# Kernel tuning notes

Hardware: AMD Instinct MI355X
Metric: run time of the kernel (lower is better)

Reference implementation:

```python
import jax, jax.numpy as jnp
import numpy as np

NUM_USERS = 100000
NUM_ITEMS = 100000
D = 128
L = 8
FV = 64
FH = 64
B = 8192
FC_IN = FV * D + FH * L  # 8704


def setup_inputs() -> dict:
    key = jax.random.key(0)
    ks = jax.random.split(key, 16)
    s = 0.05  # weight scale for sane magnitudes
    return {
        "user_id": jax.random.randint(ks[0], (B,), 0, NUM_USERS),
        "seq_L": jax.random.randint(ks[1], (B, L), 0, NUM_ITEMS),
        "item_id": jax.random.randint(ks[2], (B,), 0, NUM_ITEMS),
        "Q": jax.random.normal(ks[3], (NUM_ITEMS, D), jnp.float32) * s,
        "P": jax.random.normal(ks[4], (NUM_USERS, D), jnp.float32) * s,
        "Qp": jax.random.normal(ks[5], (NUM_ITEMS, 2 * D), jnp.float32) * s,
        "b_item": jax.random.normal(ks[6], (NUM_ITEMS,), jnp.float32) * s,
        "Wv": jax.random.normal(ks[7], (FV, L), jnp.float32) * s,
        "bv": jax.random.normal(ks[8], (FV,), jnp.float32) * s,
        "Wh": jax.random.normal(ks[9], (L, FH, L, D), jnp.float32) * s,
        "bh": jax.random.normal(ks[10], (L, FH), jnp.float32) * s,
        "Wfc": jax.random.normal(ks[11], (D, FC_IN), jnp.float32) * s,
        "bfc": jax.random.normal(ks[12], (D,), jnp.float32) * s,
    }


def reference(user_id, seq_L, item_id, Q, P, Qp, b_item, Wv, bv, Wh, bh, Wfc, bfc):
    # seq embeddings: [B, L, D]
    x = Q[seq_L]
    # vertical conv: kernel (L,1) -> out [B, Fv, D], then relu + flatten
    out_v = jax.nn.relu(jnp.einsum("bld,fl->bfd", x, Wv) + bv[None, :, None])
    out_v = out_v.reshape(out_v.shape[0], FV * D)  # [B, Fv*D]
    # horizontal conv blocks h = 1..L (static loop over kernel heights)
    h_feats = []
    for h in range(1, L + 1):
        w = Wh[h - 1, :, :h, :]  # [Fh, h, D]
        # sliding windows over sequence: [B, L-h+1, h, D]
        win = jnp.stack([x[:, j : j + h] for j in range(L - h + 1)], axis=1)
        o = jnp.einsum("bjhd,fhd->bjf", win, w) + bh[h - 1]  # [B, L-h+1, Fh]
        h_feats.append(jnp.max(jax.nn.relu(o), axis=1))  # [B, Fh]
    out_h = jnp.concatenate(h_feats, axis=1)  # [B, Fh*L]
    combined = jnp.concatenate([out_v, out_h], axis=1)  # [B, Fv*D + Fh*L]
    # (dropout p=0 / inference -> identity)
    z = jax.nn.relu(combined @ Wfc.T + bfc)  # [B, D]
    x2 = jnp.concatenate([z, P[user_id]], axis=1)  # [B, 2D]
    score = jnp.einsum("bd,bd->b", x2, Qp[item_id]) + b_item[item_id]
    return score
```

## Files before the change

### kernel.cpp

```cpp
#include <hip/hip_runtime.h>
#include <hip/hip_bf16.h>
#include <cstdint>
#include <cstddef>

typedef short bf16x8 __attribute__((ext_vector_type(8)));
typedef short bf16x4 __attribute__((ext_vector_type(4)));
typedef float f32x4  __attribute__((ext_vector_type(4)));

#define MFMA16(A, B, C) __builtin_amdgcn_mfma_f32_16x16x32_bf16(A, B, C, 0, 0, 0)

constexpr int XSTR = 1032;
constexpr int BSTR = 520;
constexpr size_t WS_FC   = (size_t)2176 * 1024;
constexpr size_t WS_BOTH = WS_FC + (size_t)576 * 1024;

__device__ __forceinline__ unsigned short f2bf(float x) {
    unsigned u = __float_as_uint(x);
    unsigned r = u + 0x7fffu + ((u >> 16) & 1u);
    return (unsigned short)(r >> 16);
}
__device__ __forceinline__ float bf2f(unsigned short h) {
    return __uint_as_float(((unsigned)h) << 16);
}
__device__ __forceinline__ unsigned pkbf(float a, float b) {
    __hip_bfloat162 h = __float22bfloat162_rn(make_float2(a, b));
    return *reinterpret_cast<unsigned*>(&h);
}
__device__ __forceinline__ bf16x8 load8_f32(const float* __restrict__ s) {
    float4 a = *(const float4*)s;
    float4 b = *(const float4*)(s + 4);
    bf16x8 r;
    r[0]=(short)f2bf(a.x); r[1]=(short)f2bf(a.y); r[2]=(short)f2bf(a.z); r[3]=(short)f2bf(a.w);
    r[4]=(short)f2bf(b.x); r[5]=(short)f2bf(b.y); r[6]=(short)f2bf(b.z); r[7]=(short)f2bf(b.w);
    return r;
}

template<int MODE>
__device__ __forceinline__ bf16x8 fc_bfrag(const unsigned short* __restrict__ wfcb,
                                           const float* __restrict__ Wfc,
                                           int kg, int ntile, int lane)
{
    if constexpr (MODE >= 1) {
        return *(const bf16x8*)(wfcb + (((size_t)(kg * 8 + ntile)) << 9) + lane * 8);
    } else {
        const float* s = Wfc + (size_t)(ntile * 16 + (lane & 15)) * 8704
                             + kg * 32 + (lane >> 4) * 8;
        return load8_f32(s);
    }
}
template<int MODE>
__device__ __forceinline__ bf16x8 wh_bfrag(const unsigned short* __restrict__ whb,
                                           const float* __restrict__ Wh,
                                           int H, int kstep, int ntile, int lane)
{
    if constexpr (MODE == 2) {
        return *(const bf16x8*)(whb +
            (((size_t)(8 * H * (H - 1) + kstep * 4 + ntile)) << 9) + lane * 8);
    } else {
        const int k = kstep * 32 + (lane >> 4) * 8;
        const float* s = Wh + ((((size_t)(H - 1) * 64 + ntile * 16 + (lane & 15)) * 8
                               + (k >> 7)) * 128 + (k & 127));
        return load8_f32(s);
    }
}

__global__ __launch_bounds__(256)
void caser_prep(const float* __restrict__ Wfc, const float* __restrict__ Wh,
                unsigned short* __restrict__ wfcb, unsigned short* __restrict__ whb,
                int nfrag)
{
    const int tid = blockIdx.x * 256 + threadIdx.x;
    const int lane = tid & 63, frag = tid >> 6;
    if (frag >= nfrag) return;
    if (frag < 2176) {
        const int kg = frag >> 3, nt = frag & 7;
        bf16x8 v = fc_bfrag<0>(nullptr, Wfc, kg, nt, lane);
        *(bf16x8*)(wfcb + ((size_t)frag << 9) + lane * 8) = v;
    } else {
        const int f2 = frag - 2176;
        int h = 1;
        while (f2 >= 8 * h * (h + 1)) ++h;
        const int fl = f2 - 8 * h * (h - 1);
        const int nt = fl & 3, kstep = fl >> 2;
        bf16x8 v = wh_bfrag<0>(nullptr, Wh, h, kstep, nt, lane);
        *(bf16x8*)(whb + ((size_t)f2 << 9) + lane * 8) = v;
    }
}

template<int H, int PP, int MODE>
__device__ __forceinline__ void hconv_compute(
    const unsigned short* __restrict__ xs,
    const unsigned short* __restrict__ whb, const float* __restrict__ Wh,
    const float* __restrict__ bh,
    int m, int nt4, int lane, int laneA, float mx[4])
{
    constexpr int NJ = 9 - H;
    constexpr int NJS = (PP == 0) ? ((NJ + 1) / 2) : (NJ / 2);
    if constexpr (NJS > 0) {
        f32x4 C[NJS] = {};
        const unsigned short* xbase = xs + m * 16 * XSTR + laneA;
        #pragma unroll
        for (int kstep = 0; kstep < 4 * H; ++kstep) {
            const int hp = kstep >> 2, d0 = (kstep & 3) * 32;
            bf16x8 B = wh_bfrag<MODE>(whb, Wh, H, kstep, nt4, lane);
            #pragma unroll
            for (int idx = 0; idx < NJS; ++idx) {
                const int j = PP + 2 * idx;
                bf16x8 A = *(const bf16x8*)(xbase + (j + hp) * 128 + d0);
                C[idx] = MFMA16(A, B, C[idx]);
            }
        }
        const float bhv = bh[(H - 1) * 64 + nt4 * 16 + (lane & 15)];
        #pragma unroll
        for (int idx = 0; idx < NJS; ++idx)
            #pragma unroll
            for (int r = 0; r < 4; ++r)
                mx[r] = fmaxf(mx[r], fmaxf(C[idx][r] + bhv, 0.f));
    }
}

template<int H, int MODE>
__device__ __forceinline__ void hstep(
    const unsigned short* __restrict__ xs, unsigned short* __restrict__ feat,
    float* __restrict__ candc,
    const unsigned short* __restrict__ whb, const float* __restrict__ Wh,
    const float* __restrict__ bh,
    int t, int lane, int laneA, int hm, int hn4, int pj)
{
    float mx[4] = {};
    if (pj == 0) hconv_compute<H, 0, MODE>(xs, whb, Wh, bh, hm, hn4, lane, laneA, mx);
    else         hconv_compute<H, 1, MODE>(xs, whb, Wh, bh, hm, hn4, lane, laneA, mx);
    #pragma unroll
    for (int r = 0; r < 4; ++r)
        candc[pj * 2176 + (hm * 16 + (lane >> 4) * 4 + r) * 68 +
              hn4 * 16 + (lane & 15)] = mx[r];
    __syncthreads();
    {
        const int s = t >> 5, f0 = (t & 31) * 2;
        float a0 = fmaxf(candc[s * 68 + f0],     candc[2176 + s * 68 + f0]);
        float a1 = fmaxf(candc[s * 68 + f0 + 1], candc[2176 + s * 68 + f0 + 1]);
        *(unsigned*)(feat + s * BSTR + (H - 1) * 64 + f0) = pkbf(a0, a1);
    }
}

template<int MODE>
__global__ __launch_bounds__(1024, 1)
void caser_main(const int* __restrict__ user_id,
                const int* __restrict__ seq,
                const int* __restrict__ item_id,
                const float* __restrict__ Q,
                const float* __restrict__ Pmat,
                const float* __restrict__ Qp,
                const float* __restrict__ b_item,
                const float* __restrict__ Wv,
                const float* __restrict__ bv,
                const float* __restrict__ Wh,
                const float* __restrict__ bh,
                const float* __restrict__ Wfc,
                const float* __restrict__ bfc,
                const unsigned short* __restrict__ wfcb,
                const unsigned short* __restrict__ whb,
                float* __restrict__ out)
{
    __shared__ unsigned short xs[32 * XSTR];
    __shared__ unsigned short fbuf[2 * 32 * BSTR];
    __shared__ float cand[2 * 32 * 68];
    __shared__ float wv_s[576];

    const int t = threadIdx.x;
    const int lane = t & 63;
    const int w = t >> 6;
    const int b0 = blockIdx.x * 32;
    const int laneA = (lane & 15) * XSTR + (lane >> 4) * 8;
    const int laneB = (lane & 15) * BSTR + (lane >> 4) * 8;
    const int kh = w & 3, ng = w >> 2;
    const int hm = w & 1, hn4 = (w >> 1) & 3, pj = (w >> 3) & 1;

    if (t < 576) wv_s[t] = (t < 512) ? Wv[t] : bv[t - 512];
    #pragma unroll
    for (int k = 0; k < 8; ++k) {
        const int idx = t + k * 1024;
        const int i = idx & 31;
        const int l = (idx >> 5) & 7;
        const int s = idx >> 8;
        const int it = seq[(b0 + s) * 8 + l];
        float4 v = *(const float4*)(Q + (size_t)it * 128 + i * 4);
        uint2 pk;
        pk.x = pkbf(v.x, v.y);
        pk.y = pkbf(v.z, v.w);
        *(uint2*)(xs + s * XSTR + l * 128 + i * 4) = pk;
    }
    __syncthreads();

    const int sv = t & 31, dq = t >> 5;
    float xr[8][4];
    #pragma unroll
    for (int l = 0; l < 8; ++l) {
        bf16x4 v = *(const bf16x4*)(xs + sv * XSTR + l * 128 + dq * 4);
        #pragma unroll
        for (int i = 0; i < 4; ++i) xr[l][i] = bf2f((unsigned short)v[i]);
    }

    f32x4 FCC[2][2] = {};

    uint2 vc[4];
    #define VCONV_HALF(hc_)                                                    \
        {                                                                      \
            _Pragma("unroll")                                                  \
            for (int fl = 0; fl < 4; ++fl) {                                   \
                const int f = (hc_) * 4 + fl;                                  \
                const float bvv = wv_s[512 + f];                               \
                float acc[4];                                                  \
                _Pragma("unroll")                                              \
                for (int i = 0; i < 4; ++i) acc[i] = bvv;                      \
                _Pragma("unroll")                                              \
                for (int l = 0; l < 8; ++l) {                                  \
                    const float wl = wv_s[f * 8 + l];                          \
                    _Pragma("unroll")                                          \
                    for (int i = 0; i < 4; ++i)                                \
                        acc[i] = fmaf(xr[l][i], wl, acc[i]);                   \
                }                                                              \
                vc[fl].x = pkbf(fmaxf(acc[0], 0.f), fmaxf(acc[1], 0.f));       \
                vc[fl].y = pkbf(fmaxf(acc[2], 0.f), fmaxf(acc[3], 0.f));       \
            }                                                                  \
        }
    #define VSTORE(buf_)                                                       \
        {                                                                      \
            unsigned short* fb = fbuf + (buf_) * (32 * BSTR);                  \
            _Pragma("unroll")                                                  \
            for (int fl = 0; fl < 4; ++fl)                                     \
                *(uint2*)(fb + sv * BSTR + fl * 128 + dq * 4) = vc[fl];        \
        }

    bf16x8 BF0[4], BF1[4];
    #pragma unroll
    for (int ks = 0; ks < 4; ++ks) {
        const int kg = kh * 4 + ks;
        BF0[ks] = fc_bfrag<MODE>(wfcb, Wfc, kg, ng * 2,     lane);
        BF1[ks] = fc_bfrag<MODE>(wfcb, Wfc, kg, ng * 2 + 1, lane);
    }
    VCONV_HALF(0);
    VSTORE(0);
    __syncthreads();

    #pragma unroll 1
    for (int hc = 0; hc < 16; ++hc) {
        {
            const unsigned short* fb = fbuf + (hc & 1) * (32 * BSTR);
            #pragma unroll
            for (int ks = 0; ks < 4; ++ks) {
                const int kl = kh * 4 + ks;
                bf16x8 A0 = *(const bf16x8*)(fb + laneB + kl * 32);
                bf16x8 A1 = *(const bf16x8*)(fb + 16 * BSTR + laneB + kl * 32);
                FCC[0][0] = MFMA16(A0, BF0[ks], FCC[0][0]);
                FCC[0][1] = MFMA16(A0, BF1[ks], FCC[0][1]);
                FCC[1][0] = MFMA16(A1, BF0[ks], FCC[1][0]);
                FCC[1][1] = MFMA16(A1, BF1[ks], FCC[1][1]);
            }
        }
        if (hc < 15) {
            #pragma unroll
            for (int ks = 0; ks < 4; ++ks) {
                const int kg = (hc + 1) * 16 + kh * 4 + ks;
                BF0[ks] = fc_bfrag<MODE>(wfcb, Wfc, kg, ng * 2,     lane);
                BF1[ks] = fc_bfrag<MODE>(wfcb, Wfc, kg, ng * 2 + 1, lane);
            }
            VCONV_HALF(hc + 1);
            VSTORE((hc + 1) & 1);
        }
        __syncthreads();
    }
    #undef VCONV_HALF
    #undef VSTORE

    unsigned short* feat = fbuf;
    float* candA = cand;
    float* candB = (float*)(fbuf + 32 * BSTR);
    hstep<1, MODE>(xs, feat, candA, whb, Wh, bh, t, lane, laneA, hm, hn4, pj);
    hstep<2, MODE>(xs, feat, candB, whb, Wh, bh, t, lane, laneA, hm, hn4, pj);
    hstep<3, MODE>(xs, feat, candA, whb, Wh, bh, t, lane, laneA, hm, hn4, pj);
    hstep<4, MODE>(xs, feat, candB, whb, Wh, bh, t, lane, laneA, hm, hn4, pj);
    hstep<5, MODE>(xs, feat, candA, whb, Wh, bh, t, lane, laneA, hm, hn4, pj);
    hstep<6, MODE>(xs, feat, candB, whb, Wh, bh, t, lane, laneA, hm, hn4, pj);
    hstep<7, MODE>(xs, feat, candA, whb, Wh, bh, t, lane, laneA, hm, hn4, pj);
    hstep<8, MODE>(xs, feat, candB, whb, Wh, bh, t, lane, laneA, hm, hn4, pj);

    #pragma unroll
    for (int kgi = 0; kgi < 4; ++kgi) {
        const int kg = 256 + kh * 4 + kgi;
        BF0[kgi] = fc_bfrag<MODE>(wfcb, Wfc, kg, ng * 2,     lane);
        BF1[kgi] = fc_bfrag<MODE>(wfcb, Wfc, kg, ng * 2 + 1, lane);
    }
    __syncthreads();

    #pragma unroll
    for (int kgi = 0; kgi < 4; ++kgi) {
        const int kloc = kh * 4 + kgi;
        bf16x8 A0 = *(const bf16x8*)(feat + laneB + kloc * 32);
        bf16x8 A1 = *(const bf16x8*)(feat + 16 * BSTR + laneB + kloc * 32);
        FCC[0][0] = MFMA16(A0, BF0[kgi], FCC[0][0]);
        FCC[0][1] = MFMA16(A0, BF1[kgi], FCC[0][1]);
        FCC[1][0] = MFMA16(A1, BF0[kgi], FCC[1][0]);
        FCC[1][1] = MFMA16(A1, BF1[kgi], FCC[1][1]);
    }

    float* zbuf4 = (float*)xs;
    #pragma unroll
    for (int m = 0; m < 2; ++m)
        #pragma unroll
        for (int nt = 0; nt < 2; ++nt)
            #pragma unroll
            for (int r = 0; r < 4; ++r)
                zbuf4[kh * (32 * 132) + (m * 16 + (lane >> 4) * 4 + r) * 132 +
                      ng * 32 + nt * 16 + (lane & 15)] = FCC[m][nt][r];
    __syncthreads();
    {
        const int s = t >> 5, l32 = t & 31, o0 = l32 * 4;
        const int b = b0 + s;
        const int item = item_id[b];
        const int user = user_id[b];
        const float* qp = Qp + (size_t)item * 256;
        const float* pu = Pmat + (size_t)user * 128;
        float acc2 = 0.f;
        #pragma unroll
        for (int i = 0; i < 4; ++i) {
            float z = zbuf4[s * 132 + o0 + i]
                    + zbuf4[1 * (32 * 132) + s * 132 + o0 + i]
                    + zbuf4[2 * (32 * 132) + s * 132 + o0 + i]
                    + zbuf4[3 * (32 * 132) + s * 132 + o0 + i]
                    + bfc[o0 + i];
            z = fmaxf(z, 0.f);
            acc2 = fmaf(z, qp[o0 + i], acc2);
        }
        #pragma unroll
        for (int i = 0; i < 4; ++i)
            acc2 = fmaf(pu[o0 + i], qp[128 + o0 + i], acc2);
        acc2 += __shfl_xor(acc2, 1, 32);
        acc2 += __shfl_xor(acc2, 2, 32);
        acc2 += __shfl_xor(acc2, 4, 32);
        acc2 += __shfl_xor(acc2, 8, 32);
        acc2 += __shfl_xor(acc2, 16, 32);
        if (l32 == 0) out[b] = acc2 + b_item[item];
    }
}

extern "C" void kernel_launch(void* const* d_in, const int* in_sizes, int n_in,
                              void* d_out, int out_size, void* d_ws, size_t ws_size,
                              hipStream_t stream)
{
    const int*   user_id = (const int*)  d_in[0];
    const int*   seq     = (const int*)  d_in[1];
    const int*   item_id = (const int*)  d_in[2];
    const float* Q       = (const float*)d_in[3];
    const float* Pmat    = (const float*)d_in[4];
    const float* Qp      = (const float*)d_in[5];
    const float* b_item  = (const float*)d_in[6];
    const float* Wv      = (const float*)d_in[7];
    const float* bv      = (const float*)d_in[8];
    const float* Wh      = (const float*)d_in[9];
    const float* bh      = (const float*)d_in[10];
    const float* Wfc     = (const float*)d_in[11];
    const float* bfc     = (const float*)d_in[12];
    float* out = (float*)d_out;

    unsigned short* wfcb = (unsigned short*)d_ws;
    unsigned short* whb  = wfcb + WS_FC / 2;

    if (ws_size >= WS_BOTH) {
        hipLaunchKernelGGL(caser_prep, dim3(688), dim3(256), 0, stream,
                           Wfc, Wh, wfcb, whb, 2752);
        hipLaunchKernelGGL((caser_main<2>), dim3(256), dim3(1024), 0, stream,
                           user_id, seq, item_id, Q, Pmat, Qp, b_item,
                           Wv, bv, Wh, bh, Wfc, bfc, wfcb, whb, out);
    } else if (ws_size >= WS_FC) {
        hipLaunchKernelGGL(caser_prep, dim3(544), dim3(256), 0, stream,
                           Wfc, Wh, wfcb, whb, 2176);
        hipLaunchKernelGGL((caser_main<1>), dim3(256), dim3(1024), 0, stream,
                           user_id, seq, item_id, Q, Pmat, Qp, b_item,
                           Wv, bv, Wh, bh, Wfc, bfc, wfcb, whb, out);
    } else {
        hipLaunchKernelGGL((caser_main<0>), dim3(256), dim3(1024), 0, stream,
                           user_id, seq, item_id, Q, Pmat, Qp, b_item,
                           Wv, bv, Wh, bh, Wfc, bfc,
                           (const unsigned short*)nullptr, (const unsigned short*)nullptr, out);
    }
}
```

Baseline: 78.44 us.

## Prefetch horizontal-conv weight fragments and pin FC fragments in registers

Restructures the horizontal conv loop to load weight fragments one kernel row at a time into a double buffer, prefetching two rows ahead, and pins FC weight fragments with empty asm so their loads land before each barrier. It also swaps the thread-to-(sample, d) mapping in the vertical conv, changing the LDS access pattern. The launch bounds now ask for 4 blocks per CU, which constrains register allocation and may cause spills in exchange for potential occupancy.

```diff
diff --git a/kernel.cpp b/kernel.cpp
--- a/kernel.cpp
+++ b/kernel.cpp
@@ -25,6 +25,9 @@
 __device__ __forceinline__ unsigned pkbf(float a, float b) {
     __hip_bfloat162 h = __float22bfloat162_rn(make_float2(a, b));
     return *reinterpret_cast<unsigned*>(&h);
+}
+__device__ __forceinline__ void pin8(bf16x8 &v) {
+    asm volatile("" : "+v"(v));
 }
 __device__ __forceinline__ bf16x8 load8_f32(const float* __restrict__ s) {
     float4 a = *(const float4*)s;
@@ -99,15 +102,33 @@
     if constexpr (NJS > 0) {
         f32x4 C[NJS] = {};
         const unsigned short* xbase = xs + m * 16 * XSTR + laneA;
-        #pragma unroll
-        for (int kstep = 0; kstep < 4 * H; ++kstep) {
-            const int hp = kstep >> 2, d0 = (kstep & 3) * 32;
-            bf16x8 B = wh_bfrag<MODE>(whb, Wh, H, kstep, nt4, lane);
-            #pragma unroll
-            for (int idx = 0; idx < NJS; ++idx) {
-                const int j = PP + 2 * idx;
-                bf16x8 A = *(const bf16x8*)(xbase + (j + hp) * 128 + d0);
-                C[idx] = MFMA16(A, B, C[idx]);
+        bf16x8 Bq[2][4];
+        #pragma unroll
+        for (int q = 0; q < 4; ++q)
+            Bq[0][q] = wh_bfrag<MODE>(whb, Wh, H, q, nt4, lane);
+        if constexpr (H > 1) {
+            #pragma unroll
+            for (int q = 0; q < 4; ++q)
+                Bq[1][q] = wh_bfrag<MODE>(whb, Wh, H, 4 + q, nt4, lane);
+        }
+        #pragma unroll
+        for (int hp = 0; hp < H; ++hp) {
+            #pragma unroll
+            for (int q = 0; q < 4; ++q) pin8(Bq[hp & 1][q]);
+            #pragma unroll
+            for (int q = 0; q < 4; ++q) {
+                const int d0 = q * 32;
+                #pragma unroll
+                for (int idx = 0; idx < NJS; ++idx) {
+                    const int j = PP + 2 * idx;
+                    bf16x8 A = *(const bf16x8*)(xbase + (j + hp) * 128 + d0);
+                    C[idx] = MFMA16(A, Bq[hp & 1][q], C[idx]);
+                }
+            }
+            if (hp + 2 < H) {
+                #pragma unroll
+                for (int q = 0; q < 4; ++q)
+                    Bq[hp & 1][q] = wh_bfrag<MODE>(whb, Wh, H, (hp + 2) * 4 + q, nt4, lane);
             }
         }
         const float bhv = bh[(H - 1) * 64 + nt4 * 16 + (lane & 15)];
@@ -144,7 +165,7 @@
 }
 
 template<int MODE>
-__global__ __launch_bounds__(1024, 1)
+__global__ __launch_bounds__(1024, 4)
 void caser_main(const int* __restrict__ user_id,
                 const int* __restrict__ seq,
                 const int* __restrict__ item_id,
@@ -192,7 +213,7 @@
     }
     __syncthreads();
 
-    const int sv = t & 31, dq = t >> 5;
+    const int sv = t >> 5, dq = t & 31;
     float xr[8][4];
     #pragma unroll
     for (int l = 0; l < 8; ++l) {
@@ -231,6 +252,11 @@
             for (int fl = 0; fl < 4; ++fl)                                     \
                 *(uint2*)(fb + sv * BSTR + fl * 128 + dq * 4) = vc[fl];        \
         }
+    #define PIN_FRAGS()                                                        \
+        {                                                                      \
+            _Pragma("unroll")                                                  \
+            for (int ks = 0; ks < 4; ++ks) { pin8(BF0[ks]); pin8(BF1[ks]); }   \
+        }
 
     bf16x8 BF0[4], BF1[4];
     #pragma unroll
@@ -241,6 +267,7 @@
     }
     VCONV_HALF(0);
     VSTORE(0);
+    PIN_FRAGS();
     __syncthreads();
 
     #pragma unroll 1
@@ -267,6 +294,7 @@
             }
             VCONV_HALF(hc + 1);
             VSTORE((hc + 1) & 1);
+            PIN_FRAGS();
         }
         __syncthreads();
     }
@@ -291,7 +319,9 @@
         BF0[kgi] = fc_bfrag<MODE>(wfcb, Wfc, kg, ng * 2,     lane);
         BF1[kgi] = fc_bfrag<MODE>(wfcb, Wfc, kg, ng * 2 + 1, lane);
     }
+    PIN_FRAGS();
     __syncthreads();
+    #undef PIN_FRAGS
 
     #pragma unroll
     for (int kgi = 0; kgi < 4; ++kgi) {
```

After: 81.86 us. 1.04x slower.

## Halve block tile to 16 rows with 512 threads and repartition FC work

Applied to the files above, without the earlier changes.

Shrinks each block from 32 to 16 batch rows and from 1024 to 512 threads, doubling the grid to 512 blocks and allowing several blocks per CU through launch bounds. The FC GEMM is repartitioned so each wave owns one 16-column output tile over the full K, instead of splitting K across four waves. This removes the cross-wave K reduction through shared memory and lets bias and ReLU be fused at the accumulator. In exchange, B fragments are loaded inside the loop without prefetch, and the Wfc weights are read by twice as many blocks.

```diff
diff --git a/kernel.cpp b/kernel.cpp
--- a/kernel.cpp
+++ b/kernel.cpp
@@ -92,13 +92,13 @@
     const unsigned short* __restrict__ xs,
     const unsigned short* __restrict__ whb, const float* __restrict__ Wh,
     const float* __restrict__ bh,
-    int m, int nt4, int lane, int laneA, float mx[4])
+    int nt4, int lane, int laneA, float mx[4])
 {
     constexpr int NJ = 9 - H;
     constexpr int NJS = (PP == 0) ? ((NJ + 1) / 2) : (NJ / 2);
     if constexpr (NJS > 0) {
         f32x4 C[NJS] = {};
-        const unsigned short* xbase = xs + m * 16 * XSTR + laneA;
+        const unsigned short* xbase = xs + laneA;
         #pragma unroll
         for (int kstep = 0; kstep < 4 * H; ++kstep) {
             const int hp = kstep >> 2, d0 = (kstep & 3) * 32;
@@ -125,26 +125,25 @@
     float* __restrict__ candc,
     const unsigned short* __restrict__ whb, const float* __restrict__ Wh,
     const float* __restrict__ bh,
-    int t, int lane, int laneA, int hm, int hn4, int pj)
+    int t, int lane, int laneA, int hn4, int pj)
 {
     float mx[4] = {};
-    if (pj == 0) hconv_compute<H, 0, MODE>(xs, whb, Wh, bh, hm, hn4, lane, laneA, mx);
-    else         hconv_compute<H, 1, MODE>(xs, whb, Wh, bh, hm, hn4, lane, laneA, mx);
+    if (pj == 0) hconv_compute<H, 0, MODE>(xs, whb, Wh, bh, hn4, lane, laneA, mx);
+    else         hconv_compute<H, 1, MODE>(xs, whb, Wh, bh, hn4, lane, laneA, mx);
     #pragma unroll
     for (int r = 0; r < 4; ++r)
-        candc[pj * 2176 + (hm * 16 + (lane >> 4) * 4 + r) * 68 +
-              hn4 * 16 + (lane & 15)] = mx[r];
+        candc[pj * 1088 + ((lane >> 4) * 4 + r) * 68 + hn4 * 16 + (lane & 15)] = mx[r];
     __syncthreads();
     {
         const int s = t >> 5, f0 = (t & 31) * 2;
-        float a0 = fmaxf(candc[s * 68 + f0],     candc[2176 + s * 68 + f0]);
-        float a1 = fmaxf(candc[s * 68 + f0 + 1], candc[2176 + s * 68 + f0 + 1]);
+        float a0 = fmaxf(candc[s * 68 + f0],     candc[1088 + s * 68 + f0]);
+        float a1 = fmaxf(candc[s * 68 + f0 + 1], candc[1088 + s * 68 + f0 + 1]);
         *(unsigned*)(feat + s * BSTR + (H - 1) * 64 + f0) = pkbf(a0, a1);
     }
 }
 
 template<int MODE>
-__global__ __launch_bounds__(1024, 1)
+__global__ __launch_bounds__(512, 4)
 void caser_main(const int* __restrict__ user_id,
                 const int* __restrict__ seq,
                 const int* __restrict__ item_id,
@@ -162,24 +161,24 @@
                 const unsigned short* __restrict__ whb,
                 float* __restrict__ out)
 {
-    __shared__ unsigned short xs[32 * XSTR];
-    __shared__ unsigned short fbuf[2 * 32 * BSTR];
-    __shared__ float cand[2 * 32 * 68];
+    __shared__ unsigned short xs[16 * XSTR];
+    __shared__ unsigned short fbuf[2 * 16 * BSTR];
+    __shared__ float cand[2 * 16 * 68];
     __shared__ float wv_s[576];
 
     const int t = threadIdx.x;
     const int lane = t & 63;
     const int w = t >> 6;
-    const int b0 = blockIdx.x * 32;
+    const int b0 = blockIdx.x * 16;
     const int laneA = (lane & 15) * XSTR + (lane >> 4) * 8;
     const int laneB = (lane & 15) * BSTR + (lane >> 4) * 8;
-    const int kh = w & 3, ng = w >> 2;
-    const int hm = w & 1, hn4 = (w >> 1) & 3, pj = (w >> 3) & 1;
-
-    if (t < 576) wv_s[t] = (t < 512) ? Wv[t] : bv[t - 512];
+    const int hn4 = w & 3, pj = w >> 2;
+
+    for (int idx = t; idx < 576; idx += 512)
+        wv_s[idx] = (idx < 512) ? Wv[idx] : bv[idx - 512];
     #pragma unroll
     for (int k = 0; k < 8; ++k) {
-        const int idx = t + k * 1024;
+        const int idx = t + k * 512;
         const int i = idx & 31;
         const int l = (idx >> 5) & 7;
         const int s = idx >> 8;
@@ -192,7 +191,7 @@
     }
     __syncthreads();
 
-    const int sv = t & 31, dq = t >> 5;
+    const int sv = t >> 5, dq = t & 31;
     float xr[8][4];
     #pragma unroll
     for (int l = 0; l < 8; ++l) {
@@ -201,7 +200,7 @@
         for (int i = 0; i < 4; ++i) xr[l][i] = bf2f((unsigned short)v[i]);
     }
 
-    f32x4 FCC[2][2] = {};
+    f32x4 FC0 = {0.f, 0.f, 0.f, 0.f}, FC1 = {0.f, 0.f, 0.f, 0.f};
 
     uint2 vc[4];
     #define VCONV_HALF(hc_)                                                    \
@@ -226,19 +225,12 @@
         }
     #define VSTORE(buf_)                                                       \
         {                                                                      \
-            unsigned short* fb = fbuf + (buf_) * (32 * BSTR);                  \
+            unsigned short* fb = fbuf + (buf_) * (16 * BSTR);                  \
             _Pragma("unroll")                                                  \
             for (int fl = 0; fl < 4; ++fl)                                     \
                 *(uint2*)(fb + sv * BSTR + fl * 128 + dq * 4) = vc[fl];        \
         }
 
-    bf16x8 BF0[4], BF1[4];
-    #pragma unroll
-    for (int ks = 0; ks < 4; ++ks) {
-        const int kg = kh * 4 + ks;
-        BF0[ks] = fc_bfrag<MODE>(wfcb, Wfc, kg, ng * 2,     lane);
-        BF1[ks] = fc_bfrag<MODE>(wfcb, Wfc, kg, ng * 2 + 1, lane);
-    }
     VCONV_HALF(0);
     VSTORE(0);
     __syncthreads();
@@ -246,25 +238,19 @@
     #pragma unroll 1
     for (int hc = 0; hc < 16; ++hc) {
         {
-            const unsigned short* fb = fbuf + (hc & 1) * (32 * BSTR);
+            const unsigned short* fb = fbuf + (hc & 1) * (16 * BSTR);
             #pragma unroll
-            for (int ks = 0; ks < 4; ++ks) {
-                const int kl = kh * 4 + ks;
-                bf16x8 A0 = *(const bf16x8*)(fb + laneB + kl * 32);
-                bf16x8 A1 = *(const bf16x8*)(fb + 16 * BSTR + laneB + kl * 32);
-                FCC[0][0] = MFMA16(A0, BF0[ks], FCC[0][0]);
-                FCC[0][1] = MFMA16(A0, BF1[ks], FCC[0][1]);
-                FCC[1][0] = MFMA16(A1, BF0[ks], FCC[1][0]);
-                FCC[1][1] = MFMA16(A1, BF1[ks], FCC[1][1]);
+            for (int ks = 0; ks < 8; ++ks) {
+                const int kl0 = 2 * ks, kl1 = 2 * ks + 1;
+                bf16x8 B0 = fc_bfrag<MODE>(wfcb, Wfc, hc * 16 + kl0, w, lane);
+                bf16x8 B1 = fc_bfrag<MODE>(wfcb, Wfc, hc * 16 + kl1, w, lane);
+                bf16x8 A0 = *(const bf16x8*)(fb + laneB + kl0 * 32);
+                bf16x8 A1 = *(const bf16x8*)(fb + laneB + kl1 * 32);
+                FC0 = MFMA16(A0, B0, FC0);
+                FC1 = MFMA16(A1, B1, FC1);
             }
         }
         if (hc < 15) {
-            #pragma unroll
-            for (int ks = 0; ks < 4; ++ks) {
-                const int kg = (hc + 1) * 16 + kh * 4 + ks;
-                BF0[ks] = fc_bfrag<MODE>(wfcb, Wfc, kg, ng * 2,     lane);
-                BF1[ks] = fc_bfrag<MODE>(wfcb, Wfc, kg, ng * 2 + 1, lane);
-            }
             VCONV_HALF(hc + 1);
             VSTORE((hc + 1) & 1);
         }
@@ -275,44 +261,38 @@
 
     unsigned short* feat = fbuf;
     float* candA = cand;
-    float* candB = (float*)(fbuf + 32 * BSTR);
-    hstep<1, MODE>(xs, feat, candA, whb, Wh, bh, t, lane, laneA, hm, hn4, pj);
-    hstep<2, MODE>(xs, feat, candB, whb, Wh, bh, t, lane, laneA, hm, hn4, pj);
-    hstep<3, MODE>(xs, feat, candA, whb, Wh, bh, t, lane, laneA, hm, hn4, pj);
-    hstep<4, MODE>(xs, feat, candB, whb, Wh, bh, t, lane, laneA, hm, hn4, pj);
-    hstep<5, MODE>(xs, feat, candA, whb, Wh, bh, t, lane, laneA, hm, hn4, pj);
-    hstep<6, MODE>(xs, feat, candB, whb, Wh, bh, t, lane, laneA, hm, hn4, pj);
-    hstep<7, MODE>(xs, feat, candA, whb, Wh, bh, t, lane, laneA, hm, hn4, pj);
-    hstep<8, MODE>(xs, feat, candB, whb, Wh, bh, t, lane, laneA, hm, hn4, pj);
+    float* candB = (float*)(fbuf + 16 * BSTR);
+    hstep<1, MODE>(xs, feat, candA, whb, Wh, bh, t, lane, laneA, hn4, pj);
+    hstep<2, MODE>(xs, feat, candB, whb, Wh, bh, t, lane, laneA, hn4, pj);
+    hstep<3, MODE>(xs, feat, candA, whb, Wh, bh, t, lane, laneA, hn4, pj);
+    hstep<4, MODE>(xs, feat, candB, whb, Wh, bh, t, lane, laneA, hn4, pj);
+    hstep<5, MODE>(xs, feat, candA, whb, Wh, bh, t, lane, laneA, hn4, pj);
+    hstep<6, MODE>(xs, feat, candB, whb, Wh, bh, t, lane, laneA, hn4, pj);
+    hstep<7, MODE>(xs, feat, candA, whb, Wh, bh, t, lane, laneA, hn4, pj);
+    hstep<8, MODE>(xs, feat, candB, whb, Wh, bh, t, lane, laneA, hn4, pj);
+    __syncthreads();
 
     #pragma unroll
-    for (int kgi = 0; kgi < 4; ++kgi) {
-        const int kg = 256 + kh * 4 + kgi;
-        BF0[kgi] = fc_bfrag<MODE>(wfcb, Wfc, kg, ng * 2,     lane);
-        BF1[kgi] = fc_bfrag<MODE>(wfcb, Wfc, kg, ng * 2 + 1, lane);
-    }
-    __syncthreads();
-
-    #pragma unroll
-    for (int kgi = 0; kgi < 4; ++kgi) {
-        const int kloc = kh * 4 + kgi;
-        bf16x8 A0 = *(const bf16x8*)(feat + laneB + kloc * 32);
-        bf16x8 A1 = *(const bf16x8*)(feat + 16 * BSTR + laneB + kloc * 32);
-        FCC[0][0] = MFMA16(A0, BF0[kgi], FCC[0][0]);
-        FCC[0][1] = MFMA16(A0, BF1[kgi], FCC[0][1]);
-        FCC[1][0] = MFMA16(A1, BF0[kgi], FCC[1][0]);
-        FCC[1][1] = MFMA16(A1, BF1[kgi], FCC[1][1]);
-    }
-
-    float* zbuf4 = (float*)xs;
-    #pragma unroll
-    for (int m = 0; m < 2; ++m)
-        #pragma unroll
-        for (int nt = 0; nt < 2; ++nt)
-            #pragma unroll
-            for (int r = 0; r < 4; ++r)
-                zbuf4[kh * (32 * 132) + (m * 16 + (lane >> 4) * 4 + r) * 132 +
-                      ng * 32 + nt * 16 + (lane & 15)] = FCC[m][nt][r];
+    for (int ks = 0; ks < 8; ++ks) {
+        const int kl0 = 2 * ks, kl1 = 2 * ks + 1;
+        bf16x8 B0 = fc_bfrag<MODE>(wfcb, Wfc, 256 + kl0, w, lane);
+        bf16x8 B1 = fc_bfrag<MODE>(wfcb, Wfc, 256 + kl1, w, lane);
+        bf16x8 A0 = *(const bf16x8*)(feat + laneB + kl0 * 32);
+        bf16x8 A1 = *(const bf16x8*)(feat + laneB + kl1 * 32);
+        FC0 = MFMA16(A0, B0, FC0);
+        FC1 = MFMA16(A1, B1, FC1);
+    }
+
+    float* zbuf = cand;
+    {
+        const int col = w * 16 + (lane & 15);
+        const float bfcv = bfc[col];
+        #pragma unroll
+        for (int r = 0; r < 4; ++r) {
+            const int row = (lane >> 4) * 4 + r;
+            zbuf[row * 132 + col] = fmaxf(FC0[r] + FC1[r] + bfcv, 0.f);
+        }
+    }
     __syncthreads();
     {
         const int s = t >> 5, l32 = t & 31, o0 = l32 * 4;
@@ -323,15 +303,8 @@
         const float* pu = Pmat + (size_t)user * 128;
         float acc2 = 0.f;
         #pragma unroll
-        for (int i = 0; i < 4; ++i) {
-            float z = zbuf4[s * 132 + o0 + i]
-                    + zbuf4[1 * (32 * 132) + s * 132 + o0 + i]
-                    + zbuf4[2 * (32 * 132) + s * 132 + o0 + i]
-                    + zbuf4[3 * (32 * 132) + s * 132 + o0 + i]
-                    + bfc[o0 + i];
-            z = fmaxf(z, 0.f);
-            acc2 = fmaf(z, qp[o0 + i], acc2);
-        }
+        for (int i = 0; i < 4; ++i)
+            acc2 = fmaf(zbuf[s * 132 + o0 + i], qp[o0 + i], acc2);
         #pragma unroll
         for (int i = 0; i < 4; ++i)
             acc2 = fmaf(pu[o0 + i], qp[128 + o0 + i], acc2);
@@ -369,17 +342,17 @@
     if (ws_size >= WS_BOTH) {
         hipLaunchKernelGGL(caser_prep, dim3(688), dim3(256), 0, stream,
                            Wfc, Wh, wfcb, whb, 2752);
-        hipLaunchKernelGGL((caser_main<2>), dim3(256), dim3(1024), 0, stream,
+        hipLaunchKernelGGL((caser_main<2>), dim3(512), dim3(512), 0, stream,
                            user_id, seq, item_id, Q, Pmat, Qp, b_item,
                            Wv, bv, Wh, bh, Wfc, bfc, wfcb, whb, out);
     } else if (ws_size >= WS_FC) {
         hipLaunchKernelGGL(caser_prep, dim3(544), dim3(256), 0, stream,
                            Wfc, Wh, wfcb, whb, 2176);
-        hipLaunchKernelGGL((caser_main<1>), dim3(256), dim3(1024), 0, stream,
+        hipLaunchKernelGGL((caser_main<1>), dim3(512), dim3(512), 0, stream,
                            user_id, seq, item_id, Q, Pmat, Qp, b_item,
                            Wv, bv, Wh, bh, Wfc, bfc, wfcb, whb, out);
     } else {
-        hipLaunchKernelGGL((caser_main<0>), dim3(256), dim3(1024), 0, stream,
+        hipLaunchKernelGGL((caser_main<0>), dim3(512), dim3(512), 0, stream,
                            user_id, seq, item_id, Q, Pmat, Qp, b_item,
                            Wv, bv, Wh, bh, Wfc, bfc,
                            (const unsigned short*)nullptr, (const unsigned short*)nullptr, out);
```

New measurement: 94.95 us. 1.21x slower.
